# Kernel tuning notes

Hardware: AMD Instinct MI355X
Metric: run time of the kernel (lower is better)

The kernel has to match this reference:

```python
import jax, jax.numpy as jnp
import numpy as np

EPS_COS = 1e-8   # torch F.cosine_similarity default eps
EPS_ADD = 1e-12  # additive eps used by the module


def setup_inputs() -> dict:
    key = jax.random.key(0)
    ks = jax.random.split(key, 7)
    B, N, M, INT_SHIFT = 1024, 4096, 64, 3
    return {
        "beta": jax.random.uniform(ks[0], (B, 1), dtype=jnp.float32),
        "kappa": jax.random.normal(ks[1], (B, M), dtype=jnp.float32),
        "gamma": jax.random.uniform(ks[2], (B, 1), dtype=jnp.float32),
        "g": jax.random.uniform(ks[3], (B, 1), dtype=jnp.float32),
        "s": jax.random.uniform(ks[4], (B, INT_SHIFT), dtype=jnp.float32),
        "w_prev": jax.random.uniform(ks[5], (B, N), dtype=jnp.float32),
        "memory": jax.random.normal(ks[6], (B, N, M), dtype=jnp.float32),
        "int_shift": INT_SHIFT,
    }


def reference(beta, kappa, gamma, g, s, w_prev, memory, int_shift):
    # --- content addressing: cosine similarity + softmax ---
    mem = memory + EPS_ADD                      # [B, N, M]
    k = kappa[:, None, :] + EPS_ADD             # [B, 1, M]
    dot = jnp.einsum('bnm,bom->bn', mem, k)     # [B, N]
    mem_norm = jnp.maximum(jnp.sqrt(jnp.sum(mem * mem, axis=-1)), EPS_COS)
    k_norm = jnp.maximum(jnp.sqrt(jnp.sum(k * k, axis=-1)), EPS_COS)  # [B, 1]
    cos = dot / (mem_norm * k_norm)             # [B, N]
    w_c = jax.nn.softmax(beta * cos, axis=1)    # beta [B,1] broadcasts

    # --- interpolate with previous weighting ---
    w_g = g * w_c + (1.0 - g) * w_prev          # [B, N]

    # --- circular shift: result[i] = sum_j w_g[(i + j - 1) mod N] * s[j] ---
    # (equivalent to the per-sample conv1d over circularly padded w_g)
    w_hat = jnp.zeros_like(w_g)
    for j in range(int_shift):
        w_hat = w_hat + s[:, j:j + 1] * jnp.roll(w_g, 1 - j, axis=1)

    # --- sharpen ---
    w = w_hat ** gamma                          # gamma [B,1]
    w = w / (jnp.sum(w, axis=1, keepdims=True) + EPS_ADD)
    return w
```

## Files before the change

kernel.cpp:

```cpp
#include <hip/hip_runtime.h>
#include <math.h>

#define EPS_COS 1e-8f
#define EPS_ADD 1e-12f

constexpr int NN = 4096;
constexpr int MM = 64;
constexpr int BLOCK = 256;

__device__ __forceinline__ float block_reduce_sum(float v, float* red) {
    #pragma unroll
    for (int o = 32; o > 0; o >>= 1) v += __shfl_xor(v, o, 64);
    const int wv = threadIdx.x >> 6;
    if ((threadIdx.x & 63) == 0) red[wv] = v;
    __syncthreads();
    float r = (red[0] + red[1]) + (red[2] + red[3]);
    __syncthreads();
    return r;
}

__global__ __launch_bounds__(BLOCK, 4) void ntm_fused(
    const float* __restrict__ beta,
    const float* __restrict__ kappa,
    const float* __restrict__ gamma_p,
    const float* __restrict__ g_p,
    const float* __restrict__ s_p,
    const float* __restrict__ w_prev,
    const float* __restrict__ memory,
    float* __restrict__ out,
    int S)
{
    const int b   = blockIdx.x;
    const int tid = threadIdx.x;
    const int sub = tid & 3;
    const int row = tid >> 2;

    __shared__ float sc[NN];
    __shared__ float red[4];

    const float beta_b  = beta[b];
    const float g_b     = g_p[b];
    const float gamma_b = gamma_p[b];
    float sreg[8];
    #pragma unroll
    for (int j = 0; j < 8; ++j) sreg[j] = (j < S) ? s_p[(size_t)b * S + j] : 0.0f;

    const float4* kv = (const float4*)(kappa + (size_t)b * MM);
    float4 kf[4];
    float ksq = 0.f;
    #pragma unroll
    for (int j = 0; j < 4; ++j) {
        float4 t = kv[sub * 4 + j];
        t.x += EPS_ADD; t.y += EPS_ADD; t.z += EPS_ADD; t.w += EPS_ADD;
        kf[j] = t;
        ksq += t.x * t.x + t.y * t.y + t.z * t.z + t.w * t.w;
    }
    ksq += __shfl_xor(ksq, 1, 64);
    ksq += __shfl_xor(ksq, 2, 64);
    const float knorm = fmaxf(sqrtf(ksq), EPS_COS);
    const float binv  = beta_b / knorm;

    float lsum = 0.f;
    const float4* memv = (const float4*)(memory + (size_t)b * NN * MM);
    #pragma unroll 2
    for (int it = 0; it < NN / 64; ++it) {
        const int n = it * 64 + row;
        const float4* rp = memv + (size_t)n * (MM / 4) + sub * 4;
        float d = 0.f, q = 0.f;
        #pragma unroll
        for (int j = 0; j < 4; ++j) {
            float4 m = rp[j];
            m.x += EPS_ADD; m.y += EPS_ADD; m.z += EPS_ADD; m.w += EPS_ADD;
            d += m.x * kf[j].x + m.y * kf[j].y + m.z * kf[j].z + m.w * kf[j].w;
            q += m.x * m.x + m.y * m.y + m.z * m.z + m.w * m.w;
        }
        d += __shfl_xor(d, 1, 64); q += __shfl_xor(q, 1, 64);
        d += __shfl_xor(d, 2, 64); q += __shfl_xor(q, 2, 64);
        if (sub == 0) {
            const float e = __expf(binv * d / fmaxf(sqrtf(q), EPS_COS));
            sc[n] = e;
            lsum += e;
        }
    }
    const float Z  = block_reduce_sum(lsum, red);
    const float gi = g_b / Z;
    const float gp = 1.0f - g_b;

    const float4* wp4 = (const float4*)(w_prev + (size_t)b * NN);
    float4* sc4 = (float4*)sc;
    #pragma unroll
    for (int k = 0; k < NN / (BLOCK * 4); ++k) {
        const int idx = tid + k * BLOCK;
        float4 e = sc4[idx];
        const float4 w = wp4[idx];
        e.x = e.x * gi + gp * w.x;
        e.y = e.y * gi + gp * w.y;
        e.z = e.z * gi + gp * w.z;
        e.w = e.w * gi + gp * w.w;
        sc4[idx] = e;
    }
    __syncthreads();

    float vals[NN / BLOCK];
    float lsum2 = 0.f;
    #pragma unroll
    for (int k = 0; k < NN / BLOCK; ++k) {
        const int n = tid + k * BLOCK;
        float acc = 0.f;
        for (int j = 0; j < S; ++j) {
            const int idx = (n + j - 1 + NN) & (NN - 1);
            acc += sreg[j] * sc[idx];
        }
        const float v = __expf(gamma_b * __logf(acc));
        vals[k] = v;
        lsum2 += v;
    }
    const float T   = block_reduce_sum(lsum2, red);
    const float inv = 1.0f / (T + EPS_ADD);
    float* outb = out + (size_t)b * NN;
    #pragma unroll
    for (int k = 0; k < NN / BLOCK; ++k) {
        outb[tid + k * BLOCK] = vals[k] * inv;
    }
}

extern "C" void kernel_launch(void* const* d_in, const int* in_sizes, int n_in,
                              void* d_out, int out_size, void* d_ws, size_t ws_size,
                              hipStream_t stream) {
    const float* beta    = (const float*)d_in[0];
    const float* kappa   = (const float*)d_in[1];
    const float* gamma_p = (const float*)d_in[2];
    const float* g_p     = (const float*)d_in[3];
    const float* s_p     = (const float*)d_in[4];
    const float* w_prev  = (const float*)d_in[5];
    const float* memory  = (const float*)d_in[6];
    float* out = (float*)d_out;

    const int B = in_sizes[0];
    int S = in_sizes[4] / B;
    if (S > 8) S = 8;

    ntm_fused<<<B, BLOCK, 0, stream>>>(beta, kappa, gamma_p, g_p, s_p,
                                       w_prev, memory, out, S);
}
```

Baseline: 197.1 us.

## Prefetch w_prev early, use nontemporal memory loads, specialize 3-tap shift path

Loads w_prev into registers, including neighbour halo elements, before the memory streaming loop so its latency overlaps the main reduction. Reads and writes the large memory tensor and the output with nontemporal builtins. Adds a specialized S==3 path that fuses interpolation, the circular 3-tap shift, sharpening and the vector store without the extra shared-memory write/sync pass. This raises register pressure and duplicates the code path.

```diff
diff --git a/kernel.cpp b/kernel.cpp
--- a/kernel.cpp
+++ b/kernel.cpp
@@ -7,6 +7,8 @@
 constexpr int NN = 4096;
 constexpr int MM = 64;
 constexpr int BLOCK = 256;
+
+using f32x4 = __attribute__((ext_vector_type(4))) float;
 
 __device__ __forceinline__ float block_reduce_sum(float v, float* red) {
     #pragma unroll
@@ -38,6 +40,17 @@
     __shared__ float sc[NN];
     __shared__ float red[4];
 
+    const float* wpb = w_prev + (size_t)b * NN;
+    f32x4 wpv[4]; float wpl[4], wpr[4];
+    #pragma unroll
+    for (int k = 0; k < 4; ++k) {
+        const int idx  = tid + k * BLOCK;
+        const int base = 4 * idx;
+        wpv[k] = ((const f32x4*)wpb)[idx];
+        wpl[k] = wpb[(base + NN - 1) & (NN - 1)];
+        wpr[k] = wpb[(base + 4) & (NN - 1)];
+    }
+
     const float beta_b  = beta[b];
     const float g_b     = g_p[b];
     const float gamma_b = gamma_p[b];
@@ -45,13 +58,13 @@
     #pragma unroll
     for (int j = 0; j < 8; ++j) sreg[j] = (j < S) ? s_p[(size_t)b * S + j] : 0.0f;
 
-    const float4* kv = (const float4*)(kappa + (size_t)b * MM);
-    float4 kf[4];
+    const f32x4* kv = (const f32x4*)(kappa + (size_t)b * MM);
+    f32x4 kf[4];
     float ksq = 0.f;
     #pragma unroll
     for (int j = 0; j < 4; ++j) {
-        float4 t = kv[sub * 4 + j];
-        t.x += EPS_ADD; t.y += EPS_ADD; t.z += EPS_ADD; t.w += EPS_ADD;
+        f32x4 t = kv[sub * 4 + j];
+        t += EPS_ADD;
         kf[j] = t;
         ksq += t.x * t.x + t.y * t.y + t.z * t.z + t.w * t.w;
     }
@@ -61,16 +74,16 @@
     const float binv  = beta_b / knorm;
 
     float lsum = 0.f;
-    const float4* memv = (const float4*)(memory + (size_t)b * NN * MM);
+    const f32x4* memv = (const f32x4*)(memory + (size_t)b * NN * MM);
     #pragma unroll 2
     for (int it = 0; it < NN / 64; ++it) {
         const int n = it * 64 + row;
-        const float4* rp = memv + (size_t)n * (MM / 4) + sub * 4;
+        const f32x4* rp = memv + (size_t)n * (MM / 4) + sub * 4;
         float d = 0.f, q = 0.f;
         #pragma unroll
         for (int j = 0; j < 4; ++j) {
-            float4 m = rp[j];
-            m.x += EPS_ADD; m.y += EPS_ADD; m.z += EPS_ADD; m.w += EPS_ADD;
+            f32x4 m = __builtin_nontemporal_load(rp + j);
+            m += EPS_ADD;
             d += m.x * kf[j].x + m.y * kf[j].y + m.z * kf[j].z + m.w * kf[j].w;
             q += m.x * m.x + m.y * m.y + m.z * m.z + m.w * m.w;
         }
@@ -86,41 +99,78 @@
     const float gi = g_b / Z;
     const float gp = 1.0f - g_b;
 
-    const float4* wp4 = (const float4*)(w_prev + (size_t)b * NN);
-    float4* sc4 = (float4*)sc;
-    #pragma unroll
-    for (int k = 0; k < NN / (BLOCK * 4); ++k) {
-        const int idx = tid + k * BLOCK;
-        float4 e = sc4[idx];
-        const float4 w = wp4[idx];
-        e.x = e.x * gi + gp * w.x;
-        e.y = e.y * gi + gp * w.y;
-        e.z = e.z * gi + gp * w.z;
-        e.w = e.w * gi + gp * w.w;
-        sc4[idx] = e;
-    }
-    __syncthreads();
+    float* outb = out + (size_t)b * NN;
 
-    float vals[NN / BLOCK];
-    float lsum2 = 0.f;
-    #pragma unroll
-    for (int k = 0; k < NN / BLOCK; ++k) {
-        const int n = tid + k * BLOCK;
-        float acc = 0.f;
-        for (int j = 0; j < S; ++j) {
-            const int idx = (n + j - 1 + NN) & (NN - 1);
-            acc += sreg[j] * sc[idx];
+    if (S == 3) {
+        const float s0 = sreg[0], s1 = sreg[1], s2 = sreg[2];
+        const f32x4* sc4 = (const f32x4*)sc;
+        f32x4 vals[4];
+        float lsum2 = 0.f;
+        #pragma unroll
+        for (int k = 0; k < 4; ++k) {
+            const int idx  = tid + k * BLOCK;
+            const int base = 4 * idx;
+            const f32x4 e  = sc4[idx];
+            const float eL = sc[(base + NN - 1) & (NN - 1)];
+            const float eR = sc[(base + 4) & (NN - 1)];
+            const float wgL = gi * eL  + gp * wpl[k];
+            const float wg0 = gi * e.x + gp * wpv[k].x;
+            const float wg1 = gi * e.y + gp * wpv[k].y;
+            const float wg2 = gi * e.z + gp * wpv[k].z;
+            const float wg3 = gi * e.w + gp * wpv[k].w;
+            const float wgR = gi * eR  + gp * wpr[k];
+            f32x4 h;
+            h.x = s0 * wgL + s1 * wg0 + s2 * wg1;
+            h.y = s0 * wg0 + s1 * wg1 + s2 * wg2;
+            h.z = s0 * wg1 + s1 * wg2 + s2 * wg3;
+            h.w = s0 * wg2 + s1 * wg3 + s2 * wgR;
+            f32x4 v;
+            v.x = __expf(gamma_b * __logf(h.x));
+            v.y = __expf(gamma_b * __logf(h.y));
+            v.z = __expf(gamma_b * __logf(h.z));
+            v.w = __expf(gamma_b * __logf(h.w));
+            vals[k] = v;
+            lsum2 += v.x + v.y + v.z + v.w;
         }
-        const float v = __expf(gamma_b * __logf(acc));
-        vals[k] = v;
-        lsum2 += v;
-    }
-    const float T   = block_reduce_sum(lsum2, red);
-    const float inv = 1.0f / (T + EPS_ADD);
-    float* outb = out + (size_t)b * NN;
-    #pragma unroll
-    for (int k = 0; k < NN / BLOCK; ++k) {
-        outb[tid + k * BLOCK] = vals[k] * inv;
+        const float T   = block_reduce_sum(lsum2, red);
+        const float inv = 1.0f / (T + EPS_ADD);
+        f32x4* out4 = (f32x4*)outb;
+        #pragma unroll
+        for (int k = 0; k < 4; ++k) {
+            __builtin_nontemporal_store(vals[k] * inv, out4 + tid + k * BLOCK);
+        }
+    } else {
+        const f32x4* wp4 = (const f32x4*)wpb;
+        f32x4* sc4 = (f32x4*)sc;
+        #pragma unroll
+        for (int k = 0; k < 4; ++k) {
+            const int idx = tid + k * BLOCK;
+            f32x4 e = sc4[idx];
+            const f32x4 w = wp4[idx];
+            e = e * gi + w * gp;
+            sc4[idx] = e;
+        }
+        __syncthreads();
+        float vals[NN / BLOCK];
+        float lsum2 = 0.f;
+        #pragma unroll
+        for (int k = 0; k < NN / BLOCK; ++k) {
+            const int n = tid + k * BLOCK;
+            float acc = 0.f;
+            for (int j = 0; j < S; ++j) {
+                const int idx = (n + j - 1 + NN) & (NN - 1);
+                acc += sreg[j] * sc[idx];
+            }
+            const float v = __expf(gamma_b * __logf(acc));
+            vals[k] = v;
+            lsum2 += v;
+        }
+        const float T   = block_reduce_sum(lsum2, red);
+        const float inv = 1.0f / (T + EPS_ADD);
+        #pragma unroll
+        for (int k = 0; k < NN / BLOCK; ++k) {
+            outb[tid + k * BLOCK] = vals[k] * inv;
+        }
     }
 }
 
```

After: 296.8 us. 1.51x slower.
